# Optimization experiments

Hardware: AMD Instinct MI355X
Metric: run time of the kernel (lower is better)

## Reference

```python
import jax, jax.numpy as jnp
import numpy as np

PH, PW = 16, 16
EMBED_DIM = 768

def setup_inputs() -> dict:
    key = jax.random.key(0)
    k1, k2, k3, k4, k5 = jax.random.split(key, 5)
    B, C, H, W = 32, 3, 384, 384
    N = 576
    x = jax.random.normal(k1, (B, C, H, W), dtype=jnp.float32)
    h_idx = jax.random.randint(k2, (B, N), 0, H - PH, dtype=jnp.int32)
    w_idx = jax.random.randint(k3, (B, N), 0, W - PW, dtype=jnp.int32)
    in_feat = PH * PW * C
    # nn.Linear default init: U(-1/sqrt(in), 1/sqrt(in))
    bound = 1.0 / np.sqrt(in_feat)
    proj_w = jax.random.uniform(k4, (EMBED_DIM, in_feat), jnp.float32, -bound, bound)
    proj_b = jax.random.uniform(k5, (EMBED_DIM,), jnp.float32, -bound, bound)
    return {"x": x, "h_idx": h_idx, "w_idx": w_idx, "proj_w": proj_w, "proj_b": proj_b}

def reference(x, h_idx, w_idx, proj_w, proj_b):
    # x: [B, C, H, W]; h_idx, w_idx: [B, N]
    B, C, H, W = x.shape
    N = h_idx.shape[1]
    rows = h_idx[:, :, None] + jnp.arange(PH, dtype=h_idx.dtype)   # [B, N, PH]
    cols = w_idx[:, :, None] + jnp.arange(PW, dtype=w_idx.dtype)   # [B, N, PW]
    xt = jnp.transpose(x, (0, 2, 3, 1))                            # [B, H, W, C]
    b_ix = jnp.arange(B)[:, None, None, None]
    # gather patches: [B, N, PH, PW, C]
    patches = xt[b_ix, rows[:, :, :, None], cols[:, :, None, :], :]
    # match torch flatten order (C, PH, PW)
    patches = jnp.transpose(patches, (0, 1, 4, 2, 3)).reshape(B, N, C * PH * PW)
    # linear projection: [B, N, E]
    return jnp.einsum('bnf,ef->bne', patches, proj_w) + proj_b
```

## Files before the change

### kernel.cpp

```cpp
#include <hip/hip_runtime.h>
#include <hip/hip_bf16.h>
#include <stdint.h>

#define B_   32
#define C_   3
#define H_   384
#define W_   384
#define N_   576
#define ED   768
#define KF   768
#define M_   (B_ * N_)

typedef __attribute__((ext_vector_type(8))) short   short8;
typedef __attribute__((ext_vector_type(8))) unsigned short ushort8;
typedef __attribute__((ext_vector_type(4))) float   f32x4;

__device__ __forceinline__ unsigned short f2bf(float f) {
    union { float f; unsigned int u; } v; v.f = f;
    unsigned int u = v.u;
    return (unsigned short)((u + 0x7FFFu + ((u >> 16) & 1u)) >> 16);
}

__global__ __launch_bounds__(256) void gather_patches(
    const float* __restrict__ x, const int* __restrict__ h_idx,
    const int* __restrict__ w_idx, unsigned short* __restrict__ Aws) {
    int gid = blockIdx.x * 256 + threadIdx.x;
    int m   = gid / 96;
    int kb  = gid - m * 96;
    int k0  = kb * 8;
    int b   = m / N_;
    int c   = k0 >> 8;
    int rem = k0 & 255;
    int ph  = rem >> 4;
    int pw  = rem & 15;
    int h = h_idx[m] + ph;
    int w = w_idx[m] + pw;
    const float* src = x + (((b * C_ + c) * H_ + h) * (long)W_ + w);
    ushort8 o;
#pragma unroll
    for (int i = 0; i < 8; ++i) o[i] = f2bf(src[i]);
    *(ushort8*)(Aws + (size_t)m * KF + k0) = o;
}

__global__ __launch_bounds__(256) void conv_w(
    const float* __restrict__ w, unsigned short* __restrict__ Wb) {
    int gid = blockIdx.x * 256 + threadIdx.x;
    const float4* s = (const float4*)w + (size_t)gid * 2;
    float4 a = s[0], bq = s[1];
    ushort8 o;
    o[0] = f2bf(a.x);  o[1] = f2bf(a.y);  o[2] = f2bf(a.z);  o[3] = f2bf(a.w);
    o[4] = f2bf(bq.x); o[5] = f2bf(bq.y); o[6] = f2bf(bq.z); o[7] = f2bf(bq.w);
    *(ushort8*)(Wb + (size_t)gid * 8) = o;
}

#define GLD16(g, l)                                                        \
    __builtin_amdgcn_global_load_lds(                                      \
        (const __attribute__((address_space(1))) unsigned int*)(g),        \
        (__attribute__((address_space(3))) unsigned int*)(l), 16, 0, 0)

__global__ __launch_bounds__(256) void gemm_bt(
    const unsigned short* __restrict__ A, const unsigned short* __restrict__ Wb,
    const float* __restrict__ bias, float* __restrict__ out) {
    __shared__ unsigned short sA[128 * 32];
    __shared__ unsigned short sB[128 * 32];

    const int t    = threadIdx.x;
    const int m0   = blockIdx.y * 128;
    const int e0   = blockIdx.x * 128;
    const int lane = t & 63;
    const int wid  = t >> 6;
    const int wr   = wid >> 1;
    const int wc   = wid & 1;
    const int r16  = lane & 15;
    const int kh   = lane >> 4;

    f32x4 acc[4][4];
#pragma unroll
    for (int i = 0; i < 4; ++i)
#pragma unroll
        for (int j = 0; j < 4; ++j) acc[i][j] = (f32x4)0.0f;

    for (int kt = 0; kt < KF / 32; ++kt) {
        const int k0 = kt * 32;
#pragma unroll
        for (int rnd = 0; rnd < 2; ++rnd) {
            const int o    = rnd * 4096 + t * 16;
            const int row  = o >> 6;
            const int cole = (o & 63) >> 1;
            GLD16(A  + (size_t)(m0 + row) * KF + k0 + cole, (char*)sA + o);
            GLD16(Wb + (size_t)(e0 + row) * KF + k0 + cole, (char*)sB + o);
        }
        __syncthreads();

        short8 af[4], bf[4];
#pragma unroll
        for (int mi = 0; mi < 4; ++mi)
            af[mi] = *(const short8*)&sA[(wr * 64 + mi * 16 + r16) * 32 + kh * 8];
#pragma unroll
        for (int ni = 0; ni < 4; ++ni)
            bf[ni] = *(const short8*)&sB[(wc * 64 + ni * 16 + r16) * 32 + kh * 8];
#pragma unroll
        for (int mi = 0; mi < 4; ++mi)
#pragma unroll
            for (int ni = 0; ni < 4; ++ni)
                acc[mi][ni] = __builtin_amdgcn_mfma_f32_16x16x32_bf16(
                    af[mi], bf[ni], acc[mi][ni], 0, 0, 0);
        __syncthreads();
    }

#pragma unroll
    for (int mi = 0; mi < 4; ++mi) {
#pragma unroll
        for (int ni = 0; ni < 4; ++ni) {
            const int ge = e0 + wc * 64 + ni * 16 + r16;
            const float bv = bias[ge];
#pragma unroll
            for (int j = 0; j < 4; ++j) {
                const int gm = m0 + wr * 64 + mi * 16 + kh * 4 + j;
                out[(size_t)gm * ED + ge] = acc[mi][ni][j] + bv;
            }
        }
    }
}

extern "C" void kernel_launch(void* const* d_in, const int* in_sizes, int n_in,
                              void* d_out, int out_size, void* d_ws, size_t ws_size,
                              hipStream_t stream) {
    const float* x      = (const float*)d_in[0];
    const int*   h_idx  = (const int*)  d_in[1];
    const int*   w_idx  = (const int*)  d_in[2];
    const float* proj_w = (const float*)d_in[3];
    const float* proj_b = (const float*)d_in[4];
    float*       out    = (float*)d_out;

    unsigned short* Aws = (unsigned short*)d_ws;
    unsigned short* Wws = Aws + (size_t)M_ * KF;

    gather_patches<<<M_ * 96 / 256, 256, 0, stream>>>(x, h_idx, w_idx, Aws);
    conv_w<<<(ED * KF / 8) / 256, 256, 0, stream>>>(proj_w, Wws);
    gemm_bt<<<dim3(ED / 128, M_ / 128), 256, 0, stream>>>(Aws, Wws, proj_b, out);
}
```

Before: 163.0 us.

## Double GEMM K-tile to 64 with XOR-swizzled LDS and block-order swizzle

```diff
diff --git a/kernel.cpp b/kernel.cpp
--- a/kernel.cpp
+++ b/kernel.cpp
@@ -58,15 +58,21 @@
         (const __attribute__((address_space(1))) unsigned int*)(g),        \
         (__attribute__((address_space(3))) unsigned int*)(l), 16, 0, 0)
 
+#define BK 64
+
 __global__ __launch_bounds__(256) void gemm_bt(
     const unsigned short* __restrict__ A, const unsigned short* __restrict__ Wb,
     const float* __restrict__ bias, float* __restrict__ out) {
-    __shared__ unsigned short sA[128 * 32];
-    __shared__ unsigned short sB[128 * 32];
+    __shared__ unsigned short sA[128 * BK];
+    __shared__ unsigned short sB[128 * BK];
 
-    const int t    = threadIdx.x;
-    const int m0   = blockIdx.y * 128;
-    const int e0   = blockIdx.x * 128;
+    const int t = threadIdx.x;
+
+    const int lin = blockIdx.y * 6 + blockIdx.x;
+    const int swz = (lin & 7) * 108 + (lin >> 3);
+    const int m0  = (swz / 6) * 128;
+    const int e0  = (swz % 6) * 128;
+
     const int lane = t & 63;
     const int wid  = t >> 6;
     const int wr   = wid >> 1;
@@ -80,31 +86,48 @@
 #pragma unroll
         for (int j = 0; j < 4; ++j) acc[i][j] = (f32x4)0.0f;
 
-    for (int kt = 0; kt < KF / 32; ++kt) {
-        const int k0 = kt * 32;
+    int st_row[4], st_gc[4];
 #pragma unroll
-        for (int rnd = 0; rnd < 2; ++rnd) {
-            const int o    = rnd * 4096 + t * 16;
-            const int row  = o >> 6;
-            const int cole = (o & 63) >> 1;
-            GLD16(A  + (size_t)(m0 + row) * KF + k0 + cole, (char*)sA + o);
-            GLD16(Wb + (size_t)(e0 + row) * KF + k0 + cole, (char*)sB + o);
+    for (int r = 0; r < 4; ++r) {
+        const int o   = r * 4096 + t * 16;
+        const int row = o >> 7;
+        const int s   = (o >> 4) & 7;
+        st_row[r] = row;
+        st_gc[r]  = (s ^ (row & 7)) * 8;
+    }
+
+    for (int kt = 0; kt < KF / BK; ++kt) {
+        const int k0 = kt * BK;
+#pragma unroll
+        for (int r = 0; r < 4; ++r) {
+            const int o = r * 4096 + t * 16;
+            GLD16(A  + (size_t)(m0 + st_row[r]) * KF + k0 + st_gc[r], (char*)sA + o);
+            GLD16(Wb + (size_t)(e0 + st_row[r]) * KF + k0 + st_gc[r], (char*)sB + o);
         }
         __syncthreads();
 
-        short8 af[4], bf[4];
 #pragma unroll
-        for (int mi = 0; mi < 4; ++mi)
-            af[mi] = *(const short8*)&sA[(wr * 64 + mi * 16 + r16) * 32 + kh * 8];
+        for (int kk = 0; kk < 2; ++kk) {
+            short8 af[4], bf[4];
 #pragma unroll
-        for (int ni = 0; ni < 4; ++ni)
-            bf[ni] = *(const short8*)&sB[(wc * 64 + ni * 16 + r16) * 32 + kh * 8];
+            for (int mi = 0; mi < 4; ++mi) {
+                const int ar = wr * 64 + mi * 16 + r16;
+                const int sl = ((kk << 2) + kh) ^ (ar & 7);
+                af[mi] = *(const short8*)&sA[ar * BK + sl * 8];
+            }
 #pragma unroll
-        for (int mi = 0; mi < 4; ++mi)
+            for (int ni = 0; ni < 4; ++ni) {
+                const int br = wc * 64 + ni * 16 + r16;
+                const int sl = ((kk << 2) + kh) ^ (br & 7);
+                bf[ni] = *(const short8*)&sB[br * BK + sl * 8];
+            }
 #pragma unroll
-            for (int ni = 0; ni < 4; ++ni)
-                acc[mi][ni] = __builtin_amdgcn_mfma_f32_16x16x32_bf16(
-                    af[mi], bf[ni], acc[mi][ni], 0, 0, 0);
+            for (int mi = 0; mi < 4; ++mi)
+#pragma unroll
+                for (int ni = 0; ni < 4; ++ni)
+                    acc[mi][ni] = __builtin_amdgcn_mfma_f32_16x16x32_bf16(
+                        af[mi], bf[ni], acc[mi][ni], 0, 0, 0);
+        }
         __syncthreads();
     }
 
```

New measurement: 153.2 us. 1.06x faster.
